# Kernel optimization log

Hardware: AMD Instinct MI355X
Metric: run time of the kernel (lower is better)

The kernel has to match this reference:

```python
import jax, jax.numpy as jnp
import numpy as np

B, N, D_MODEL, H, D_K, D_V = 2, 2048, 1024, 16, 64, 64


def setup_inputs() -> dict:
    key = jax.random.key(0)
    ks = jax.random.split(key, 8)
    queries = jax.random.normal(ks[0], (B, N, D_MODEL), dtype=jnp.float32)
    keys = jax.random.normal(ks[1], (B, N, D_MODEL), dtype=jnp.float32)
    values = jax.random.normal(ks[2], (B, N, D_MODEL), dtype=jnp.float32)
    # nn.Linear weights: (out_features, in_features); init.normal_(std=0.001) in the
    # original, but we use a larger scale for a numerically meaningful test.
    Wq = jax.random.normal(ks[3], (H * D_K, D_MODEL), dtype=jnp.float32) * 0.02
    Wk = jax.random.normal(ks[4], (H * D_K, D_MODEL), dtype=jnp.float32) * 0.02
    Wv = jax.random.normal(ks[5], (H * D_V, D_MODEL), dtype=jnp.float32) * 0.02
    Wo = jax.random.normal(ks[6], (D_MODEL, H * D_V), dtype=jnp.float32) * 0.02
    bo = jnp.zeros((D_MODEL,), dtype=jnp.float32)
    return {"queries": queries, "keys": keys, "values": values,
            "Wq": Wq, "Wk": Wk, "Wv": Wv, "Wo": Wo, "bo": bo}


def reference(queries, keys, values, Wq, Wk, Wv, Wo, bo):
    b, nq, _ = queries.shape
    nk = keys.shape[1]
    scale = 1.0 / np.sqrt(D_K).astype(np.float32)
    # projections: (b, n, h, d)
    q = (queries @ Wq.T).reshape(b, nq, H, D_K)
    k = (keys @ Wk.T).reshape(b, nk, H, D_K)
    v = (values @ Wv.T).reshape(b, nk, H, D_V)
    # scaled dot-product attention; seq_mask=None, attention_weights=None, dropout p=0
    att = jnp.einsum('bqhd,bkhd->bhqk', q, k) * scale  # (b, h, nq, nk)
    att = jax.nn.softmax(att, axis=-1)
    out = jnp.einsum('bhqk,bkhd->bqhd', att, v).reshape(b, nq, H * D_V)
    return queries + (out @ Wo.T + bo)
```

## Files before the change

### kernel.cpp

```cpp
#include <hip/hip_runtime.h>
#include <hip/hip_bf16.h>
#include <stdint.h>

#define BATCH  2
#define SEQ    2048
#define DMODEL 1024
#define NHEAD  16
#define DHEAD  64

typedef unsigned short u16;
typedef __attribute__((ext_vector_type(8))) short bf16x8;
typedef __attribute__((ext_vector_type(4))) float f32x4;

__device__ __forceinline__ u16 f2bf(float x) {
    union { float f; uint32_t u; } v; v.f = x;
    uint32_t r = v.u + 0x7fffu + ((v.u >> 16) & 1u);
    return (u16)(r >> 16);
}

__device__ __forceinline__ uint32_t pk2bf(float a, float b) {
    __hip_bfloat162 h = __float22bfloat162_rn(make_float2(a, b));
    return *(uint32_t*)&h;
}

__device__ __forceinline__ float exp2_raw(float x) {
    float r;
    asm("v_exp_f32 %0, %1" : "=v"(r) : "v"(x));
    return r;
}

__device__ __forceinline__ void gload_lds16(const void* g, void* l) {
    __builtin_amdgcn_global_load_lds(
        (const __attribute__((address_space(1))) uint32_t*)(uintptr_t)g,
        (__attribute__((address_space(3))) uint32_t*)(uintptr_t)l,
        16, 0, 0);
}

__device__ __forceinline__ f32x4 mfma16(bf16x8 a, bf16x8 b, f32x4 c) {
    return __builtin_amdgcn_mfma_f32_16x16x32_bf16(a, b, c, 0, 0, 0);
}

__global__ __launch_bounds__(256) void cvt4_kernel(
    const float* s0, const float* s1, const float* s2, const float* s3,
    u16* d0, u16* d1, u16* d2, u16* d3)
{
    const float* s; u16* d;
    switch (blockIdx.y) {
        case 0: s = s0; d = d0; break;
        case 1: s = s1; d = d1; break;
        case 2: s = s2; d = d2; break;
        default: s = s3; d = d3; break;
    }
    size_t i = ((size_t)blockIdx.x * 256 + threadIdx.x) * 8;
    float4 a = *(const float4*)(s + i);
    float4 b = *(const float4*)(s + i + 4);
    union { uint4 v; u16 e[8]; } u;
    u.e[0] = f2bf(a.x); u.e[1] = f2bf(a.y); u.e[2] = f2bf(a.z); u.e[3] = f2bf(a.w);
    u.e[4] = f2bf(b.x); u.e[5] = f2bf(b.y); u.e[6] = f2bf(b.z); u.e[7] = f2bf(b.w);
    *(uint4*)(d + i) = u.v;
}

__device__ __forceinline__ void gemm_core_128_f32A(
    const float* __restrict__ A, const u16* __restrict__ Bm, int K,
    int brow, int bcol, u16* As, u16* Bs, f32x4 (&acc)[4][4])
{
    const int tid  = threadIdx.x;
    const int lane = tid & 63;
    const int wr   = ((tid >> 6) >> 1) * 64;
    const int wc   = ((tid >> 6) & 1) * 64;
    const int srow = tid >> 2;
    const int scol = (tid & 3) * 8;
    const int fr   = lane & 15;
    const int fk   = (lane >> 4) * 8;

    for (int k0 = 0; k0 < K; k0 += 32) {
        {
            const float* s0 = A + (size_t)(brow + srow) * K + k0 + scol;
            const float* s1 = A + (size_t)(brow + 64 + srow) * K + k0 + scol;
            float4 a0 = *(const float4*)(s0);
            float4 a1 = *(const float4*)(s0 + 4);
            float4 b0 = *(const float4*)(s1);
            float4 b1 = *(const float4*)(s1 + 4);
            uint4 wA, wB;
            wA.x = pk2bf(a0.x, a0.y); wA.y = pk2bf(a0.z, a0.w);
            wA.z = pk2bf(a1.x, a1.y); wA.w = pk2bf(a1.z, a1.w);
            wB.x = pk2bf(b0.x, b0.y); wB.y = pk2bf(b0.z, b0.w);
            wB.z = pk2bf(b1.x, b1.y); wB.w = pk2bf(b1.z, b1.w);
            *(uint4*)(As + srow * 32 + scol) = wA;
            *(uint4*)(As + (64 + srow) * 32 + scol) = wB;
        }
        gload_lds16(Bm + (size_t)(bcol + srow) * K + k0 + scol,       Bs + srow * 32 + scol);
        gload_lds16(Bm + (size_t)(bcol + 64 + srow) * K + k0 + scol,  Bs + (64 + srow) * 32 + scol);
        __syncthreads();
        bf16x8 af[4], bfv[4];
        #pragma unroll
        for (int i = 0; i < 4; ++i) {
            af[i]  = *(const bf16x8*)(As + (wr + i * 16 + fr) * 32 + fk);
            bfv[i] = *(const bf16x8*)(Bs + (wc + i * 16 + fr) * 32 + fk);
        }
        #pragma unroll
        for (int am = 0; am < 4; ++am)
            #pragma unroll
            for (int bn = 0; bn < 4; ++bn)
                acc[am][bn] = mfma16(af[am], bfv[bn], acc[am][bn]);
        __syncthreads();
    }
}

__device__ __forceinline__ void gemm_core_64x128(
    const u16* __restrict__ A, const u16* __restrict__ Bm, int K,
    int brow, int bcol, u16* As, u16* Bs, f32x4 (&acc)[4][2])
{
    const int tid  = threadIdx.x;
    const int lane = tid & 63;
    const int wc   = (tid >> 6) * 32;
    const int srow = tid >> 2;
    const int scol = (tid & 3) * 8;
    const int fr   = lane & 15;
    const int fk   = (lane >> 4) * 8;

    for (int k0 = 0; k0 < K; k0 += 32) {
        gload_lds16(A  + (size_t)(brow + srow) * K + k0 + scol,       As + srow * 32 + scol);
        gload_lds16(Bm + (size_t)(bcol + srow) * K + k0 + scol,       Bs + srow * 32 + scol);
        gload_lds16(Bm + (size_t)(bcol + 64 + srow) * K + k0 + scol,  Bs + (64 + srow) * 32 + scol);
        __syncthreads();
        bf16x8 af[4], bfv[2];
        #pragma unroll
        for (int i = 0; i < 4; ++i)
            af[i]  = *(const bf16x8*)(As + (i * 16 + fr) * 32 + fk);
        #pragma unroll
        for (int i = 0; i < 2; ++i)
            bfv[i] = *(const bf16x8*)(Bs + (wc + i * 16 + fr) * 32 + fk);
        #pragma unroll
        for (int am = 0; am < 4; ++am)
            #pragma unroll
            for (int bn = 0; bn < 2; ++bn)
                acc[am][bn] = mfma16(af[am], bfv[bn], acc[am][bn]);
        __syncthreads();
    }
}

__global__ __launch_bounds__(256) void gemm_qkv_kernel(
    const float* __restrict__ Xq, const float* __restrict__ Xk, const float* __restrict__ Xv,
    const u16* __restrict__ Wq, const u16* __restrict__ Wk, const u16* __restrict__ Wv,
    u16* __restrict__ Qo, u16* __restrict__ Ko, u16* __restrict__ Vt,
    int M, int Nn, int K)
{
    __shared__ u16 As[128 * 32];
    __shared__ u16 Bs[128 * 32];
    const int z = blockIdx.z;
    const float* A = (z == 0) ? Xq : (z == 1) ? Xk : Xv;
    const u16* Bm  = (z == 0) ? Wq : (z == 1) ? Wk : Wv;
    const float scale = (z == 0) ? 0.18033688011112042f : 1.0f;

    const int lin  = blockIdx.y * gridDim.x + blockIdx.x;
    const int nlin = (lin & 7) * 32 + (lin >> 3);
    const int brow = (nlin >> 3) * 128;
    const int bcol = (nlin & 7) * 128;
    f32x4 acc[4][4];
    #pragma unroll
    for (int am = 0; am < 4; ++am)
        #pragma unroll
        for (int bn = 0; bn < 4; ++bn)
            acc[am][bn] = (f32x4){0.f, 0.f, 0.f, 0.f};

    gemm_core_128_f32A(A, Bm, K, brow, bcol, As, Bs, acc);

    const int lane = threadIdx.x & 63;
    const int wr = ((threadIdx.x >> 6) >> 1) * 64;
    const int wc = ((threadIdx.x >> 6) & 1) * 64;
    const int fr = lane & 15;
    const int fj4 = (lane >> 4) * 4;

    if (z == 2) {
        #pragma unroll
        for (int am = 0; am < 4; ++am)
            #pragma unroll
            for (int bn = 0; bn < 4; ++bn) {
                int row = brow + wr + am * 16 + fj4;
                int col = bcol + wc + bn * 16 + fr;
                int b   = row >> 11;
                int n   = row & 2047;
                int h   = col >> 6;
                int d   = col & 63;
                uint2 w;
                w.x = pk2bf(acc[am][bn][0], acc[am][bn][1]);
                w.y = pk2bf(acc[am][bn][2], acc[am][bn][3]);
                *(uint2*)(Vt + ((size_t)(b * 16 + h) * DHEAD + d) * SEQ + n) = w;
            }
    } else {
        u16* D = (z == 0) ? Qo : Ko;
        #pragma unroll
        for (int am = 0; am < 4; ++am)
            #pragma unroll
            for (int bn = 0; bn < 4; ++bn)
                #pragma unroll
                for (int j = 0; j < 4; ++j) {
                    int row = brow + wr + am * 16 + fj4 + j;
                    int col = bcol + wc + bn * 16 + fr;
                    D[(size_t)row * Nn + col] = f2bf(acc[am][bn][j] * scale);
                }
    }
}

__global__ __launch_bounds__(256, 2) void gemm_out_kernel(
    const u16* __restrict__ A, const u16* __restrict__ Bm,
    const float* __restrict__ bias, const float* __restrict__ resid,
    float* __restrict__ D, int M, int Nn, int K)
{
    __shared__ u16 As[64 * 32];
    __shared__ u16 Bs[128 * 32];

    const int lin  = blockIdx.y * gridDim.x + blockIdx.x;
    const int nlin = (lin & 7) * 64 + (lin >> 3);
    const int brow = (nlin >> 3) * 64;
    const int bcol = (nlin & 7) * 128;
    f32x4 acc[4][2];
    #pragma unroll
    for (int am = 0; am < 4; ++am)
        #pragma unroll
        for (int bn = 0; bn < 2; ++bn)
            acc[am][bn] = (f32x4){0.f, 0.f, 0.f, 0.f};

    gemm_core_64x128(A, Bm, K, brow, bcol, As, Bs, acc);

    const int lane = threadIdx.x & 63;
    const int wc = (threadIdx.x >> 6) * 32;
    const int fr = lane & 15;
    const int fj4 = (lane >> 4) * 4;
    #pragma unroll
    for (int am = 0; am < 4; ++am)
        #pragma unroll
        for (int bn = 0; bn < 2; ++bn)
            #pragma unroll
            for (int j = 0; j < 4; ++j) {
                int row = brow + am * 16 + fj4 + j;
                int col = bcol + wc + bn * 16 + fr;
                D[(size_t)row * Nn + col] = acc[am][bn][j] + bias[col] + resid[(size_t)row * Nn + col];
            }
}

__global__ __launch_bounds__(1024, 1) void attn_kernel(
    const u16* __restrict__ Qb, const u16* __restrict__ Kb, const u16* __restrict__ Vt,
    u16* __restrict__ AO)
{
    __shared__ u16 Ks[3][64 * 64];
    __shared__ u16 Vs[3][64 * 64];
    __shared__ u16 Ps[256 * 72];

    const int tid  = threadIdx.x;
    const int lane = tid & 63;
    const int wave = tid >> 6;

    const int lin  = blockIdx.x;
    const int nlin = (lin & 7) * 32 + (lin >> 3);
    const int qblk = nlin & 7;
    const int bh   = nlin >> 3;

    const size_t rowbase = (size_t)(bh >> 4) * SEQ;
    const int colbase = (bh & 15) * DHEAD;
    const int q0 = qblk * 256;
    const int fr  = lane & 15;
    const int g   = lane >> 4;
    const int fk  = g * 8;
    const int fj4 = g * 4;
    const int qw  = wave * 16;

    const u16* Kh = Kb + rowbase * DMODEL + colbase;
    const u16* Vh = Vt + (size_t)bh * DHEAD * SEQ;

    const int st  = tid & 511;
    const int sr  = st >> 3;
    const int sc  = st & 7;
    const int scs = (sc ^ (sr & 7)) << 3;
    const int sdst = sr * 64 + sc * 8;
    const bool stageK = (tid < 512);

    bf16x8 qf[2];
    #pragma unroll
    for (int kc = 0; kc < 2; ++kc)
        qf[kc] = *(const bf16x8*)(Qb + (rowbase + q0 + qw + fr) * DMODEL
                                     + colbase + kc * 32 + fk);

    f32x4 oacc[4];
    float lsum = 0.f;
    #pragma unroll
    for (int dn = 0; dn < 4; ++dn) oacc[dn] = (f32x4){0.f, 0.f, 0.f, 0.f};

    if (stageK) {
        gload_lds16(Kh + (size_t)sr * DMODEL + scs,        &Ks[0][sdst]);
        gload_lds16(Kh + (size_t)(64 + sr) * DMODEL + scs, &Ks[1][sdst]);
    } else {
        gload_lds16(Vh + (size_t)sr * SEQ + scs,           &Vs[0][sdst]);
        gload_lds16(Vh + (size_t)sr * SEQ + 64 + scs,      &Vs[1][sdst]);
    }

    const int NT = SEQ / 64;
    int cur = 0;
    for (int t = 0; t < NT; ++t) {
        if (t < NT - 1) {
            asm volatile("s_waitcnt vmcnt(1)" ::: "memory");
        } else {
            asm volatile("s_waitcnt vmcnt(0)" ::: "memory");
        }
        __builtin_amdgcn_s_barrier();
        __builtin_amdgcn_sched_barrier(0);

        if (t + 2 < NT) {
            int wbuf = cur + 2; if (wbuf >= 3) wbuf -= 3;
            const size_t kvn = (size_t)(t + 2) * 64;
            if (stageK) gload_lds16(Kh + (kvn + sr) * DMODEL + scs,    &Ks[wbuf][sdst]);
            else        gload_lds16(Vh + (size_t)sr * SEQ + kvn + scs, &Vs[wbuf][sdst]);
        }

        const u16* K0 = &Ks[cur][0];
        const u16* V0 = &Vs[cur][0];

        f32x4 sacc[4];
        #pragma unroll
        for (int bn = 0; bn < 4; ++bn) sacc[bn] = (f32x4){0.f, 0.f, 0.f, 0.f};
        __builtin_amdgcn_s_setprio(1);
        #pragma unroll
        for (int bn = 0; bn < 4; ++bn) {
            bf16x8 kf0 = *(const bf16x8*)(K0 + (bn * 16 + fr) * 64 + (((g)     ^ (fr & 7)) << 3));
            bf16x8 kf1 = *(const bf16x8*)(K0 + (bn * 16 + fr) * 64 + (((4 + g) ^ (fr & 7)) << 3));
            sacc[bn] = mfma16(kf0, qf[0], sacc[bn]);
            sacc[bn] = mfma16(kf1, qf[1], sacc[bn]);
        }
        __builtin_amdgcn_s_setprio(0);

        {
            float lacc = 0.f;
            #pragma unroll
            for (int bn = 0; bn < 4; ++bn) {
                float p0 = exp2_raw(sacc[bn][0]);
                float p1 = exp2_raw(sacc[bn][1]);
                float p2 = exp2_raw(sacc[bn][2]);
                float p3 = exp2_raw(sacc[bn][3]);
                uint2 w;
                w.x = pk2bf(p0, p1);
                w.y = pk2bf(p2, p3);
                *(uint2*)(Ps + (qw + fr) * 72 + bn * 16 + fj4) = w;
                lacc += (p0 + p1) + (p2 + p3);
            }
            lsum += lacc;
        }

        bf16x8 pf[2];
        #pragma unroll
        for (int kc = 0; kc < 2; ++kc)
            pf[kc] = *(const bf16x8*)(Ps + (qw + fr) * 72 + kc * 32 + fk);
        __builtin_amdgcn_s_setprio(1);
        #pragma unroll
        for (int dn = 0; dn < 4; ++dn) {
            bf16x8 vf0 = *(const bf16x8*)(V0 + (dn * 16 + fr) * 64 + (((g)     ^ (fr & 7)) << 3));
            bf16x8 vf1 = *(const bf16x8*)(V0 + (dn * 16 + fr) * 64 + (((4 + g) ^ (fr & 7)) << 3));
            oacc[dn] = mfma16(pf[0], vf0, oacc[dn]);
            oacc[dn] = mfma16(pf[1], vf1, oacc[dn]);
        }
        __builtin_amdgcn_s_setprio(0);

        cur = (cur == 2) ? 0 : cur + 1;
    }

    float invj[4];
    {
        float l = lsum;
        l += __shfl_xor(l, 16);
        l += __shfl_xor(l, 32);
        #pragma unroll
        for (int j = 0; j < 4; ++j) {
            float lj = __shfl(l, (lane & 48) | (fj4 + j));
            invj[j] = 1.f / lj;
        }
    }

    #pragma unroll
    for (int dn = 0; dn < 4; ++dn)
        #pragma unroll
        for (int j = 0; j < 4; ++j) {
            int row = q0 + qw + fj4 + j;
            AO[(rowbase + row) * DMODEL + colbase + dn * 16 + fr] =
                f2bf(oacc[dn][j] * invj[j]);
        }
}

extern "C" void kernel_launch(void* const* d_in, const int* in_sizes, int n_in,
                              void* d_out, int out_size, void* d_ws, size_t ws_size,
                              hipStream_t stream)
{
    const float* q_f  = (const float*)d_in[0];
    const float* k_f  = (const float*)d_in[1];
    const float* v_f  = (const float*)d_in[2];
    const float* Wq_f = (const float*)d_in[3];
    const float* Wk_f = (const float*)d_in[4];
    const float* Wv_f = (const float*)d_in[5];
    const float* Wo_f = (const float*)d_in[6];
    const float* bo_f = (const float*)d_in[7];

    char* ws = (char*)d_ws;
    const size_t ACT = (size_t)BATCH * SEQ * DMODEL * sizeof(u16);
    const size_t WSZ = (size_t)DMODEL * DMODEL * sizeof(u16);
    u16* Wqb = (u16*)(ws);
    u16* Wkb = (u16*)(ws + WSZ);
    u16* Wvb = (u16*)(ws + 2 * WSZ);
    u16* Wob = (u16*)(ws + 3 * WSZ);
    u16* Qb  = (u16*)(ws + 4 * WSZ);
    u16* Kb  = (u16*)(ws + 4 * WSZ + ACT);
    u16* Vt  = (u16*)(ws + 4 * WSZ + 2 * ACT);
    u16* AO  = (u16*)(ws + 4 * WSZ + 3 * ACT);

    const int M = BATCH * SEQ;
    const int Nn = DMODEL;
    const int K = DMODEL;

    cvt4_kernel<<<dim3(512, 4, 1), 256, 0, stream>>>(
        Wq_f, Wk_f, Wv_f, Wo_f, Wqb, Wkb, Wvb, Wob);

    gemm_qkv_kernel<<<dim3(Nn / 128, M / 128, 3), 256, 0, stream>>>(
        q_f, k_f, v_f, Wqb, Wkb, Wvb, Qb, Kb, Vt, M, Nn, K);

    attn_kernel<<<dim3(256, 1, 1), 1024, 0, stream>>>(Qb, Kb, Vt, AO);

    gemm_out_kernel<<<dim3(Nn / 128, M / 64, 1), 256, 0, stream>>>(
        AO, Wob, bo_f, q_f, (float*)d_out, M, Nn, K);
}
```

Measured before the change: 120.3 us.

## Triple-buffer QKV GEMM with async fp32 A loads to LDS and swizzle

The QKV projection GEMM now streams the fp32 activation tile directly into LDS with async global-to-LDS loads, using an XOR swizzle, and converts it to bf16 when reading fragments. A three-slot ring buffer prefetches two K-tiles ahead, using vmcnt waits and a single barrier per iteration, and raises wave priority around the MFMA block. This aims to hide global load latency and remove the register round-trip of the fp32 conversion. In exchange it uses much more LDS (about 72KB per block), which can lower occupancy, and it repeats the conversion work for each wave that reads the same rows.

```diff
diff --git a/kernel.cpp b/kernel.cpp
--- a/kernel.cpp
+++ b/kernel.cpp
@@ -60,9 +60,10 @@
     *(uint4*)(d + i) = u.v;
 }
 
-__device__ __forceinline__ void gemm_core_128_f32A(
+__device__ __forceinline__ void gemm_core_128_f32lds(
     const float* __restrict__ A, const u16* __restrict__ Bm, int K,
-    int brow, int bcol, u16* As, u16* Bs, f32x4 (&acc)[4][4])
+    int brow, int bcol, float (&As)[3][128 * 32], u16 (&Bs)[3][128 * 32],
+    f32x4 (&acc)[4][4])
 {
     const int tid  = threadIdx.x;
     const int lane = tid & 63;
@@ -71,40 +72,72 @@
     const int srow = tid >> 2;
     const int scol = (tid & 3) * 8;
     const int fr   = lane & 15;
-    const int fk   = (lane >> 4) * 8;
-
-    for (int k0 = 0; k0 < K; k0 += 32) {
-        {
-            const float* s0 = A + (size_t)(brow + srow) * K + k0 + scol;
-            const float* s1 = A + (size_t)(brow + 64 + srow) * K + k0 + scol;
-            float4 a0 = *(const float4*)(s0);
-            float4 a1 = *(const float4*)(s0 + 4);
-            float4 b0 = *(const float4*)(s1);
-            float4 b1 = *(const float4*)(s1 + 4);
-            uint4 wA, wB;
-            wA.x = pk2bf(a0.x, a0.y); wA.y = pk2bf(a0.z, a0.w);
-            wA.z = pk2bf(a1.x, a1.y); wA.w = pk2bf(a1.z, a1.w);
-            wB.x = pk2bf(b0.x, b0.y); wB.y = pk2bf(b0.z, b0.w);
-            wB.z = pk2bf(b1.x, b1.y); wB.w = pk2bf(b1.z, b1.w);
-            *(uint4*)(As + srow * 32 + scol) = wA;
-            *(uint4*)(As + (64 + srow) * 32 + scol) = wB;
-        }
-        gload_lds16(Bm + (size_t)(bcol + srow) * K + k0 + scol,       Bs + srow * 32 + scol);
-        gload_lds16(Bm + (size_t)(bcol + 64 + srow) * K + k0 + scol,  Bs + (64 + srow) * 32 + scol);
-        __syncthreads();
+    const int g    = lane >> 4;
+    const int fk   = g * 8;
+
+    const int NT = K / 32;
+
+    #define STAGE_QKV(slot, k0)                                                   \
+        {                                                                         \
+            _Pragma("unroll")                                                     \
+            for (int i = 0; i < 4; ++i) {                                         \
+                int ch = tid + i * 256;                                           \
+                int ar = ch >> 3;                                                 \
+                int ac = ch & 7;                                                  \
+                gload_lds16(A + (size_t)(brow + ar) * K + (k0) +                  \
+                                ((ac ^ (ar & 7)) << 2),                           \
+                            &As[slot][ar * 32 + ac * 4]);                         \
+            }                                                                     \
+            gload_lds16(Bm + (size_t)(bcol + srow) * K + (k0) + scol,             \
+                        &Bs[slot][srow * 32 + scol]);                             \
+            gload_lds16(Bm + (size_t)(bcol + 64 + srow) * K + (k0) + scol,        \
+                        &Bs[slot][(64 + srow) * 32 + scol]);                      \
+        }
+
+    STAGE_QKV(0, 0)
+    STAGE_QKV(1, 32)
+
+    int cur = 0;
+    for (int t = 0; t < NT; ++t) {
+        if (t < NT - 1) {
+            asm volatile("s_waitcnt vmcnt(6)" ::: "memory");
+        } else {
+            asm volatile("s_waitcnt vmcnt(0)" ::: "memory");
+        }
+        __builtin_amdgcn_s_barrier();
+        __builtin_amdgcn_sched_barrier(0);
+
+        if (t + 2 < NT) {
+            int wbuf = cur + 2; if (wbuf >= 3) wbuf -= 3;
+            STAGE_QKV(wbuf, (t + 2) * 32)
+        }
+
+        const float* A0 = &As[cur][0];
+        const u16*   B0 = &Bs[cur][0];
+
         bf16x8 af[4], bfv[4];
         #pragma unroll
         for (int i = 0; i < 4; ++i) {
-            af[i]  = *(const bf16x8*)(As + (wr + i * 16 + fr) * 32 + fk);
-            bfv[i] = *(const bf16x8*)(Bs + (wc + i * 16 + fr) * 32 + fk);
-        }
+            int r = wr + i * 16 + fr;
+            f32x4 v0 = *(const f32x4*)(A0 + r * 32 + (((2 * g)     ^ (fr & 7)) << 2));
+            f32x4 v1 = *(const f32x4*)(A0 + r * 32 + (((2 * g + 1) ^ (fr & 7)) << 2));
+            union { bf16x8 v; uint32_t u[4]; } w;
+            w.u[0] = pk2bf(v0[0], v0[1]); w.u[1] = pk2bf(v0[2], v0[3]);
+            w.u[2] = pk2bf(v1[0], v1[1]); w.u[3] = pk2bf(v1[2], v1[3]);
+            af[i] = w.v;
+            bfv[i] = *(const bf16x8*)(B0 + (wc + i * 16 + fr) * 32 + fk);
+        }
+        __builtin_amdgcn_s_setprio(1);
         #pragma unroll
         for (int am = 0; am < 4; ++am)
             #pragma unroll
             for (int bn = 0; bn < 4; ++bn)
                 acc[am][bn] = mfma16(af[am], bfv[bn], acc[am][bn]);
-        __syncthreads();
-    }
+        __builtin_amdgcn_s_setprio(0);
+
+        cur = (cur == 2) ? 0 : cur + 1;
+    }
+    #undef STAGE_QKV
 }
 
 __device__ __forceinline__ void gemm_core_64x128(
@@ -146,8 +179,8 @@
     u16* __restrict__ Qo, u16* __restrict__ Ko, u16* __restrict__ Vt,
     int M, int Nn, int K)
 {
-    __shared__ u16 As[128 * 32];
-    __shared__ u16 Bs[128 * 32];
+    __shared__ float As[3][128 * 32];
+    __shared__ u16   Bs[3][128 * 32];
     const int z = blockIdx.z;
     const float* A = (z == 0) ? Xq : (z == 1) ? Xk : Xv;
     const u16* Bm  = (z == 0) ? Wq : (z == 1) ? Wk : Wv;
@@ -164,7 +197,7 @@
         for (int bn = 0; bn < 4; ++bn)
             acc[am][bn] = (f32x4){0.f, 0.f, 0.f, 0.f};
 
-    gemm_core_128_f32A(A, Bm, K, brow, bcol, As, Bs, acc);
+    gemm_core_128_f32lds(A, Bm, K, brow, bcol, As, Bs, acc);
 
     const int lane = threadIdx.x & 63;
     const int wr = ((threadIdx.x >> 6) >> 1) * 64;
@@ -417,11 +450,11 @@
     cvt4_kernel<<<dim3(512, 4, 1), 256, 0, stream>>>(
         Wq_f, Wk_f, Wv_f, Wo_f, Wqb, Wkb, Wvb, Wob);
 
-    gemm_qkv_kernel<<<dim3(Nn / 128, M / 128, 3), 256, 0, stream>>>(
+    gemm_qkv_kernel<<<dim3(8, 32, 3), 256, 0, stream>>>(
         q_f, k_f, v_f, Wqb, Wkb, Wvb, Qb, Kb, Vt, M, Nn, K);
 
     attn_kernel<<<dim3(256, 1, 1), 1024, 0, stream>>>(Qb, Kb, Vt, AO);
 
-    gemm_out_kernel<<<dim3(Nn / 128, M / 64, 1), 256, 0, stream>>>(
+    gemm_out_kernel<<<dim3(8, 64, 1), 256, 0, stream>>>(
         AO, Wob, bo_f, q_f, (float*)d_out, M, Nn, K);
 }
```

Result: slower. 125.9 us (+4.6%).
